# Kernel tuning notes

Hardware: AMD Instinct MI355X
Metric: run time of the kernel (lower is better)

The kernel has to match this reference:

```python
import jax, jax.numpy as jnp
import numpy as np

N = 100000      # nodes
E = 1600000     # edges
D = 64          # in_dim (node/edge feature dim)
H = 128         # hidden = 2*in_dim (num_layers=2 MLP)
OUT = 64        # out_dim
EPS = 1e-7      # GENConv eps
BN_EPS = 1e-5   # BatchNorm1d eps
NORM_EPS = 1e-12  # F.normalize eps


def setup_inputs() -> dict:
    key = jax.random.key(0)
    ks = jax.random.split(key, 10)
    feats = jax.random.normal(ks[0], (N, D), dtype=jnp.float32)
    edge_h = jax.random.normal(ks[1], (E, D), dtype=jnp.float32)
    src = jax.random.randint(ks[2], (E,), 0, N, dtype=jnp.int32)
    dst = jax.random.randint(ks[3], (E,), 0, N, dtype=jnp.int32)
    # MLP params: Linear(D,H) -> BN(H) -> ReLU -> Linear(H,OUT)
    W1 = jax.random.normal(ks[4], (D, H), dtype=jnp.float32) * 0.05
    b1 = jnp.zeros((H,), dtype=jnp.float32)
    gamma = jnp.ones((H,), dtype=jnp.float32)
    bn_beta = jnp.zeros((H,), dtype=jnp.float32)
    W2 = jax.random.normal(ks[5], (H, OUT), dtype=jnp.float32) * 0.05
    b2 = jnp.zeros((OUT,), dtype=jnp.float32)
    scale = jnp.ones((1,), dtype=jnp.float32)  # MessageNorm scale (not learned)
    return {"feats": feats, "edge_h": edge_h, "src": src, "dst": dst,
            "W1": W1, "b1": b1, "gamma": gamma, "bn_beta": bn_beta,
            "W2": W2, "b2": b2, "scale": scale}


def reference(feats, edge_h, W1, b1, gamma, bn_beta, W2, b2, scale, src, dst):
    beta = 1.0
    # message: m = relu(x_src + e) + eps            [E, D]
    m = jax.nn.relu(feats[src] + edge_h) + EPS
    # edge_softmax over incoming edges of each dst node (per feature channel)
    logits = m * beta
    gmax = jax.ops.segment_max(logits, dst, num_segments=N)   # [N, D]
    ex = jnp.exp(logits - gmax[dst])                          # [E, D]
    den = jax.ops.segment_sum(ex, dst, num_segments=N)        # [N, D]
    a = ex / den[dst]
    # weighted scatter-sum aggregation
    h = jax.ops.segment_sum(m * a, dst, num_segments=N)       # [N, D]
    # MessageNorm: feats + normalize(msg) * ||feats||_2 * scale
    feat_norm = jnp.linalg.norm(feats, axis=-1, keepdims=True)
    msg_norm = jnp.linalg.norm(h, axis=-1, keepdims=True)
    msg = h / jnp.maximum(msg_norm, NORM_EPS)
    x = feats + msg * feat_norm * scale
    # MLP: Linear -> BatchNorm1d (training-mode batch stats) -> ReLU -> Linear
    x = x @ W1 + b1
    mean = jnp.mean(x, axis=0)
    var = jnp.mean(jnp.square(x - mean), axis=0)  # biased, as torch BN
    x = (x - mean) * jax.lax.rsqrt(var + BN_EPS) * gamma + bn_beta
    x = jax.nn.relu(x)
    return x @ W2 + b2
```

## Files before the change

kernel.cpp:

```cpp
#include <hip/hip_runtime.h>
#include <cstdint>

#define N_NODES 100000
#define E_EDGES 1600000
#define D_IN 64
#define H_DIM 128
#define OUT_DIM 64
#define EPS_GEN 1e-7f
#define BN_EPS 1e-5f
#define NORM_EPS 1e-12f

#define NBUCKET 391
#define P1_CHUNK 4096

typedef int ivec4 __attribute__((ext_vector_type(4)));

__global__ __launch_bounds__(256) void hist_kernel(
    const int* __restrict__ dst, int* __restrict__ counts)
{
    int t = blockIdx.x * 256 + threadIdx.x;
    if (t < E_EDGES / 4) {
        ivec4 d = __builtin_nontemporal_load((const ivec4*)dst + t);
        atomicAdd(&counts[d.x], 1);
        atomicAdd(&counts[d.y], 1);
        atomicAdd(&counts[d.z], 1);
        atomicAdd(&counts[d.w], 1);
    }
}

__global__ __launch_bounds__(256) void scan1(
    const int* __restrict__ counts, int* __restrict__ row_start,
    int* __restrict__ bsum)
{
    __shared__ int s[256];
    int t = threadIdx.x, g = blockIdx.x * 256 + t;
    int v = (g < N_NODES) ? counts[g] : 0;
    s[t] = v;
    __syncthreads();
    #pragma unroll
    for (int off = 1; off < 256; off <<= 1) {
        int u = (t >= off) ? s[t - off] : 0;
        __syncthreads();
        s[t] += u;
        __syncthreads();
    }
    if (g < N_NODES) row_start[g] = s[t];
    if (t == 255) bsum[blockIdx.x] = s[255];
}

__global__ __launch_bounds__(512) void scan2(int* __restrict__ bsum, int nb)
{
    __shared__ int s[512];
    int t = threadIdx.x;
    int v = (t < nb) ? bsum[t] : 0;
    s[t] = v;
    __syncthreads();
    #pragma unroll
    for (int off = 1; off < 512; off <<= 1) {
        int u = (t >= off) ? s[t - off] : 0;
        __syncthreads();
        s[t] += u;
        __syncthreads();
    }
    if (t < nb) bsum[t] = s[t] - v;
}

__global__ __launch_bounds__(256) void scan3b(
    const int* __restrict__ counts, const int* __restrict__ bsum,
    int* __restrict__ row_start, int* __restrict__ bcur)
{
    int g = blockIdx.x * 256 + threadIdx.x;
    if (g < N_NODES) {
        int incl = row_start[g];
        int rs = incl - counts[g] + bsum[blockIdx.x];
        row_start[g] = rs;
        if ((g & 255) == 0) bcur[g >> 8] = rs;
    }
    if (g == 0) row_start[N_NODES] = E_EDGES;
}

__global__ __launch_bounds__(256) void bin_p1(
    const int* __restrict__ dst, const int* __restrict__ src,
    int* __restrict__ bcur, unsigned long long* __restrict__ binned)
{
    __shared__ unsigned long long buf[P1_CHUNK];
    __shared__ int cnt[NBUCKET];
    __shared__ int base_l[NBUCKET];
    __shared__ int pos[NBUCKET];
    __shared__ int gb[NBUCKET];
    __shared__ int s[256];
    int tid = threadIdx.x;
    long e0 = (long)blockIdx.x * P1_CHUNK;

    for (int b = tid; b < NBUCKET; b += 256) cnt[b] = 0;
    __syncthreads();
    for (int i = tid; i < P1_CHUNK; i += 256) {
        long e = e0 + i;
        if (e < E_EDGES) atomicAdd(&cnt[dst[e] >> 8], 1);
    }
    __syncthreads();
    int a0 = (2 * tid     < NBUCKET) ? cnt[2 * tid]     : 0;
    int a1 = (2 * tid + 1 < NBUCKET) ? cnt[2 * tid + 1] : 0;
    s[tid] = a0 + a1;
    __syncthreads();
    #pragma unroll
    for (int off = 1; off < 256; off <<= 1) {
        int u = (tid >= off) ? s[tid - off] : 0;
        __syncthreads();
        s[tid] += u;
        __syncthreads();
    }
    int pb = s[tid] - a0 - a1;
    if (2 * tid < NBUCKET)     { base_l[2 * tid] = pb;          pos[2 * tid] = pb; }
    if (2 * tid + 1 < NBUCKET) { base_l[2 * tid + 1] = pb + a0; pos[2 * tid + 1] = pb + a0; }
    __syncthreads();
    for (int i = tid; i < P1_CHUNK; i += 256) {
        long e = e0 + i;
        if (e < E_EDGES) {
            int d = dst[e], sr = src[e];
            int b = d >> 8;
            int p = atomicAdd(&pos[b], 1);
            buf[p] = ((unsigned long long)(d & 255) << 38)
                   | ((unsigned long long)(unsigned)sr << 21)
                   | (unsigned long long)e;
        }
    }
    __syncthreads();
    for (int b = tid; b < NBUCKET; b += 256) {
        int c = cnt[b];
        gb[b] = c ? atomicAdd(&bcur[b], c) : 0;
    }
    __syncthreads();
    int wv = tid >> 6, ln = tid & 63;
    for (int b = wv; b < NBUCKET; b += 4) {
        int c = cnt[b];
        if (!c) continue;
        int lb = base_l[b], g = gb[b];
        for (int i = ln; i < c; i += 64)
            binned[(size_t)g + i] = buf[lb + i];
    }
}

__global__ __launch_bounds__(256) void sort_p2(
    const unsigned long long* __restrict__ binned,
    const int* __restrict__ row_start, int2* __restrict__ adj)
{
    __shared__ int ncur[256];
    int b = blockIdx.x, tid = threadIdx.x;
    int node_base = b << 8;
    int nn = min(256, N_NODES - node_base);
    int base = row_start[node_base];
    int count = row_start[min(node_base + 256, N_NODES)] - base;
    if (tid < nn) ncur[tid] = row_start[node_base + tid] - base;
    __syncthreads();
    for (int i = tid; i < count; i += 256) {
        unsigned long long v = __builtin_nontemporal_load(&binned[(size_t)base + i]);
        int dl  = (int)(v >> 38);
        int p   = atomicAdd(&ncur[dl], 1);
        int eid = (int)(v & 0x1FFFFFull);
        int sr  = (int)((v >> 21) & 0x1FFFFull);
        adj[(size_t)base + p] = make_int2(eid, sr);
    }
}

__global__ __launch_bounds__(256) void aggregate(
    const float* __restrict__ feats, const float* __restrict__ edge_h,
    const int2* __restrict__ adj, const int* __restrict__ row_start,
    const float* __restrict__ scale, float* __restrict__ x)
{
    int node = blockIdx.x * 4 + (threadIdx.x >> 6);
    int lane = threadIdx.x & 63;
    if (node >= N_NODES) return;
    int rs = row_start[node], re = row_start[node + 1];
    float den = 0.f, hn = 0.f;

    for (int base = rs; base < re; base += 64) {
        int rem = min(64, re - base);
        int2 ad = make_int2(0, 0);
        if (base + lane < re) {
            unsigned long long v = __builtin_nontemporal_load(
                (const unsigned long long*)&adj[base + lane]);
            ad.x = (int)(unsigned)v;
            ad.y = (int)(unsigned)(v >> 32);
        }
        for (int j = 0; j < rem; j += 8) {
            #pragma unroll
            for (int u = 0; u < 8; u++) {
                int jj = j + u;
                int eid = __shfl(ad.x, jj);
                int sid = __shfl(ad.y, jj);
                float fv = feats[(size_t)sid * D_IN + lane];
                float ev = __builtin_nontemporal_load(
                               &edge_h[(size_t)eid * D_IN + lane]);
                float m = fmaxf(fv + ev, 0.f) + EPS_GEN;
                float ex = __expf(m);
                bool ok = jj < rem;
                den += ok ? ex : 0.f;
                hn  += ok ? m * ex : 0.f;
            }
        }
    }

    float h = den > 0.f ? hn / den : 0.f;
    float f = feats[(size_t)node * D_IN + lane];
    float s1 = h * h, s2 = f * f;
    #pragma unroll
    for (int off = 32; off > 0; off >>= 1) {
        s1 += __shfl_xor(s1, off, 64);
        s2 += __shfl_xor(s2, off, 64);
    }
    float xv = f + (h / fmaxf(sqrtf(s1), NORM_EPS)) * sqrtf(s2) * scale[0];
    x[(size_t)node * D_IN + lane] = xv;
}

__global__ __launch_bounds__(256) void gemm1_stats(
    const float* __restrict__ x, const float* __restrict__ W1,
    const float* __restrict__ b1, float* __restrict__ y1,
    float* __restrict__ stats)
{
    __shared__ float wlds[D_IN * H_DIM];
    __shared__ float ssum[H_DIM], ssq[H_DIM];
    int tid = threadIdx.x;
    {
        const float4* wg = (const float4*)W1;
        float4* wl = (float4*)wlds;
        #pragma unroll
        for (int i = 0; i < 8; i++) wl[tid + i * 256] = wg[tid + i * 256];
    }
    if (tid < H_DIM) { ssum[tid] = 0.f; ssq[tid] = 0.f; }
    __syncthreads();

    int rg = tid >> 5, cg = tid & 31;
    int r0 = blockIdx.x * 32 + rg * 4;
    int c0 = cg * 4;
    float acc[4][4];
    {
        float4 bb = *(const float4*)(b1 + c0);
        #pragma unroll
        for (int i = 0; i < 4; i++) {
            acc[i][0] = bb.x; acc[i][1] = bb.y; acc[i][2] = bb.z; acc[i][3] = bb.w;
        }
    }
    #pragma unroll 2
    for (int kc = 0; kc < D_IN; kc += 4) {
        float4 xr[4];
        #pragma unroll
        for (int i = 0; i < 4; i++) {
            int r = r0 + i;
            xr[i] = (r < N_NODES) ? *(const float4*)(x + (size_t)r * D_IN + kc)
                                  : make_float4(0.f, 0.f, 0.f, 0.f);
        }
        #pragma unroll
        for (int kk = 0; kk < 4; kk++) {
            float4 w4 = *(const float4*)&wlds[(kc + kk) * H_DIM + c0];
            #pragma unroll
            for (int i = 0; i < 4; i++) {
                float xv = ((const float*)&xr[i])[kk];
                acc[i][0] = fmaf(xv, w4.x, acc[i][0]);
                acc[i][1] = fmaf(xv, w4.y, acc[i][1]);
                acc[i][2] = fmaf(xv, w4.z, acc[i][2]);
                acc[i][3] = fmaf(xv, w4.w, acc[i][3]);
            }
        }
    }
    float cs[4] = {0.f, 0.f, 0.f, 0.f}, cq[4] = {0.f, 0.f, 0.f, 0.f};
    #pragma unroll
    for (int i = 0; i < 4; i++) {
        int r = r0 + i;
        if (r < N_NODES) {
            *(float4*)(y1 + (size_t)r * H_DIM + c0) =
                make_float4(acc[i][0], acc[i][1], acc[i][2], acc[i][3]);
            #pragma unroll
            for (int j = 0; j < 4; j++) {
                cs[j] += acc[i][j];
                cq[j] += acc[i][j] * acc[i][j];
            }
        }
    }
    #pragma unroll
    for (int j = 0; j < 4; j++) {
        atomicAdd(&ssum[c0 + j], cs[j]);
        atomicAdd(&ssq[c0 + j], cq[j]);
    }
    __syncthreads();
    if (tid < H_DIM) {
        unsafeAtomicAdd(&stats[tid], ssum[tid]);
        unsafeAtomicAdd(&stats[H_DIM + tid], ssq[tid]);
    }
}

__global__ __launch_bounds__(256) void gemm2_bn(
    const float* __restrict__ y1, const float* __restrict__ W2,
    const float* __restrict__ b2, const float* __restrict__ stats,
    const float* __restrict__ gamma, const float* __restrict__ beta,
    float* __restrict__ out)
{
    __shared__ float wlds[H_DIM * OUT_DIM];
    __shared__ float sc[H_DIM], sh[H_DIM];
    int tid = threadIdx.x;
    {
        const float4* wg = (const float4*)W2;
        float4* wl = (float4*)wlds;
        #pragma unroll
        for (int i = 0; i < 8; i++) wl[tid + i * 256] = wg[tid + i * 256];
    }
    if (tid < H_DIM) {
        float mean = stats[tid] * (1.f / N_NODES);
        float var  = stats[H_DIM + tid] * (1.f / N_NODES) - mean * mean;
        float rs   = rsqrtf(var + BN_EPS);
        float s    = gamma[tid] * rs;
        sc[tid] = s;
        sh[tid] = beta[tid] - mean * s;
    }
    __syncthreads();

    int rg = tid >> 4, cg = tid & 15;
    int r0 = blockIdx.x * 64 + rg * 4;
    int c0 = cg * 4;
    float acc[4][4];
    {
        float4 bb = *(const float4*)(b2 + c0);
        #pragma unroll
        for (int i = 0; i < 4; i++) {
            acc[i][0] = bb.x; acc[i][1] = bb.y; acc[i][2] = bb.z; acc[i][3] = bb.w;
        }
    }
    #pragma unroll 2
    for (int kc = 0; kc < H_DIM; kc += 4) {
        float4 sc4 = *(const float4*)&sc[kc];
        float4 sh4 = *(const float4*)&sh[kc];
        float4 yr[4];
        #pragma unroll
        for (int i = 0; i < 4; i++) {
            int r = r0 + i;
            if (r < N_NODES) {
                float4 v = *(const float4*)(y1 + (size_t)r * H_DIM + kc);
                v.x = fmaxf(fmaf(v.x, sc4.x, sh4.x), 0.f);
                v.y = fmaxf(fmaf(v.y, sc4.y, sh4.y), 0.f);
                v.z = fmaxf(fmaf(v.z, sc4.z, sh4.z), 0.f);
                v.w = fmaxf(fmaf(v.w, sc4.w, sh4.w), 0.f);
                yr[i] = v;
            } else {
                yr[i] = make_float4(0.f, 0.f, 0.f, 0.f);
            }
        }
        #pragma unroll
        for (int kk = 0; kk < 4; kk++) {
            float4 w4 = *(const float4*)&wlds[(kc + kk) * OUT_DIM + c0];
            #pragma unroll
            for (int i = 0; i < 4; i++) {
                float yv = ((const float*)&yr[i])[kk];
                acc[i][0] = fmaf(yv, w4.x, acc[i][0]);
                acc[i][1] = fmaf(yv, w4.y, acc[i][1]);
                acc[i][2] = fmaf(yv, w4.z, acc[i][2]);
                acc[i][3] = fmaf(yv, w4.w, acc[i][3]);
            }
        }
    }
    #pragma unroll
    for (int i = 0; i < 4; i++) {
        int r = r0 + i;
        if (r < N_NODES) {
            *(float4*)(out + (size_t)r * OUT_DIM + c0) =
                make_float4(acc[i][0], acc[i][1], acc[i][2], acc[i][3]);
        }
    }
}

extern "C" void kernel_launch(void* const* d_in, const int* in_sizes, int n_in,
                              void* d_out, int out_size, void* d_ws, size_t ws_size,
                              hipStream_t stream)
{
    const float* feats   = (const float*)d_in[0];
    const float* edge_h  = (const float*)d_in[1];
    const int*   src     = (const int*)d_in[2];
    const int*   dst     = (const int*)d_in[3];
    const float* W1      = (const float*)d_in[4];
    const float* b1      = (const float*)d_in[5];
    const float* gamma   = (const float*)d_in[6];
    const float* bn_beta = (const float*)d_in[7];
    const float* W2      = (const float*)d_in[8];
    const float* b2      = (const float*)d_in[9];
    const float* scale   = (const float*)d_in[10];
    float* out = (float*)d_out;

    const size_t ND = (size_t)N_NODES * D_IN;
    char* ws = (char*)d_ws;
    int*   counts    = (int*)ws;                          ws += (size_t)N_NODES * 4;
    float* stats     = (float*)ws;                        ws += 256 * 4;
    int*   bsum      = (int*)ws;                          ws += 512 * 4;
    int*   row_start = (int*)ws;                          ws += (size_t)(N_NODES + 1) * 4;
    int*   bcur      = (int*)ws;                          ws += 512 * 4;
    unsigned long long* binned = (unsigned long long*)ws; ws += (size_t)E_EDGES * 8;
    int2*  adj       = (int2*)ws;                         ws += (size_t)E_EDGES * 8;
    float* xbuf      = (float*)ws;                        ws += ND * 4;
    float* y1        = (float*)ws;

    const int NB  = (N_NODES + 255) / 256;
    const int EB4 = (E_EDGES / 4 + 255) / 256;
    const int P1B = (E_EDGES + P1_CHUNK - 1) / P1_CHUNK;

    hipMemsetAsync(counts, 0, (size_t)(N_NODES + 256) * 4, stream);

    hist_kernel<<<EB4, 256, 0, stream>>>(dst, counts);
    scan1<<<NB, 256, 0, stream>>>(counts, row_start, bsum);
    scan2<<<1, 512, 0, stream>>>(bsum, NB);
    scan3b<<<NB, 256, 0, stream>>>(counts, bsum, row_start, bcur);
    bin_p1<<<P1B, 256, 0, stream>>>(dst, src, bcur, binned);
    sort_p2<<<NBUCKET, 256, 0, stream>>>(binned, row_start, adj);
    aggregate<<<(N_NODES + 3) / 4, 256, 0, stream>>>(feats, edge_h, adj, row_start, scale, xbuf);
    gemm1_stats<<<(N_NODES + 31) / 32, 256, 0, stream>>>(xbuf, W1, b1, y1, stats);
    gemm2_bn<<<(N_NODES + 63) / 64, 256, 0, stream>>>(y1, W2, b2, stats, gamma, bn_beta, out);
}
```

Before: 887.6 us.

## Replace per-node histogram and scan with bucket-level counts, derive row starts in sort

The global per-node histogram with atomics and the three-kernel scan are replaced by a per-bucket histogram kept in shared memory plus a single small scan. Per-node row starts are now computed inside sort_p2 by a local count and scan over each bucket's binned entries. bin_p1 also loads dst and src as int4 vectors, and its write-out is reworked to use a binary search per element instead of a per-bucket wave loop. The aim is fewer launches and fewer global atomics in CSR construction, at the cost of an extra pass over binned data in sort_p2 and the binary-search overhead.

```diff
diff --git a/kernel.cpp b/kernel.cpp
--- a/kernel.cpp
+++ b/kernel.cpp
@@ -15,44 +15,33 @@
 
 typedef int ivec4 __attribute__((ext_vector_type(4)));
 
-__global__ __launch_bounds__(256) void hist_kernel(
-    const int* __restrict__ dst, int* __restrict__ counts)
-{
-    int t = blockIdx.x * 256 + threadIdx.x;
-    if (t < E_EDGES / 4) {
-        ivec4 d = __builtin_nontemporal_load((const ivec4*)dst + t);
-        atomicAdd(&counts[d.x], 1);
-        atomicAdd(&counts[d.y], 1);
-        atomicAdd(&counts[d.z], 1);
-        atomicAdd(&counts[d.w], 1);
-    }
-}
-
-__global__ __launch_bounds__(256) void scan1(
-    const int* __restrict__ counts, int* __restrict__ row_start,
-    int* __restrict__ bsum)
-{
-    __shared__ int s[256];
-    int t = threadIdx.x, g = blockIdx.x * 256 + t;
-    int v = (g < N_NODES) ? counts[g] : 0;
-    s[t] = v;
-    __syncthreads();
-    #pragma unroll
-    for (int off = 1; off < 256; off <<= 1) {
-        int u = (t >= off) ? s[t - off] : 0;
-        __syncthreads();
-        s[t] += u;
-        __syncthreads();
-    }
-    if (g < N_NODES) row_start[g] = s[t];
-    if (t == 255) bsum[blockIdx.x] = s[255];
-}
-
-__global__ __launch_bounds__(512) void scan2(int* __restrict__ bsum, int nb)
+__global__ __launch_bounds__(256) void bucket_hist(
+    const int* __restrict__ dst, int* __restrict__ bc)
+{
+    __shared__ int c[NBUCKET];
+    int tid = threadIdx.x;
+    int e0 = blockIdx.x * P1_CHUNK;
+    int total = min(P1_CHUNK, E_EDGES - e0);
+    for (int b = tid; b < NBUCKET; b += 256) c[b] = 0;
+    __syncthreads();
+    for (int i4 = tid; i4 * 4 < total; i4 += 256) {
+        ivec4 d = __builtin_nontemporal_load((const ivec4*)(dst + e0) + i4);
+        atomicAdd(&c[d.x >> 8], 1);
+        atomicAdd(&c[d.y >> 8], 1);
+        atomicAdd(&c[d.z >> 8], 1);
+        atomicAdd(&c[d.w >> 8], 1);
+    }
+    __syncthreads();
+    for (int b = tid; b < NBUCKET; b += 256)
+        if (c[b]) atomicAdd(&bc[b], c[b]);
+}
+
+__global__ __launch_bounds__(512) void bucket_scan(
+    const int* __restrict__ bc, int* __restrict__ bbase, int* __restrict__ bcur)
 {
     __shared__ int s[512];
     int t = threadIdx.x;
-    int v = (t < nb) ? bsum[t] : 0;
+    int v = (t < NBUCKET) ? bc[t] : 0;
     s[t] = v;
     __syncthreads();
     #pragma unroll
@@ -62,21 +51,12 @@
         s[t] += u;
         __syncthreads();
     }
-    if (t < nb) bsum[t] = s[t] - v;
-}
-
-__global__ __launch_bounds__(256) void scan3b(
-    const int* __restrict__ counts, const int* __restrict__ bsum,
-    int* __restrict__ row_start, int* __restrict__ bcur)
-{
-    int g = blockIdx.x * 256 + threadIdx.x;
-    if (g < N_NODES) {
-        int incl = row_start[g];
-        int rs = incl - counts[g] + bsum[blockIdx.x];
-        row_start[g] = rs;
-        if ((g & 255) == 0) bcur[g >> 8] = rs;
-    }
-    if (g == 0) row_start[N_NODES] = E_EDGES;
+    if (t < NBUCKET) {
+        int ex = s[t] - v;
+        bbase[t] = ex;
+        bcur[t]  = ex;
+    }
+    if (t == 0) bbase[NBUCKET] = E_EDGES;
 }
 
 __global__ __launch_bounds__(256) void bin_p1(
@@ -90,13 +70,17 @@
     __shared__ int gb[NBUCKET];
     __shared__ int s[256];
     int tid = threadIdx.x;
-    long e0 = (long)blockIdx.x * P1_CHUNK;
+    int e0 = blockIdx.x * P1_CHUNK;
+    int total = min(P1_CHUNK, E_EDGES - e0);
 
     for (int b = tid; b < NBUCKET; b += 256) cnt[b] = 0;
     __syncthreads();
-    for (int i = tid; i < P1_CHUNK; i += 256) {
-        long e = e0 + i;
-        if (e < E_EDGES) atomicAdd(&cnt[dst[e] >> 8], 1);
+    for (int i4 = tid; i4 * 4 < total; i4 += 256) {
+        ivec4 d = ((const ivec4*)(dst + e0))[i4];
+        atomicAdd(&cnt[d.x >> 8], 1);
+        atomicAdd(&cnt[d.y >> 8], 1);
+        atomicAdd(&cnt[d.z >> 8], 1);
+        atomicAdd(&cnt[d.w >> 8], 1);
     }
     __syncthreads();
     int a0 = (2 * tid     < NBUCKET) ? cnt[2 * tid]     : 0;
@@ -114,51 +98,77 @@
     if (2 * tid < NBUCKET)     { base_l[2 * tid] = pb;          pos[2 * tid] = pb; }
     if (2 * tid + 1 < NBUCKET) { base_l[2 * tid + 1] = pb + a0; pos[2 * tid + 1] = pb + a0; }
     __syncthreads();
-    for (int i = tid; i < P1_CHUNK; i += 256) {
-        long e = e0 + i;
-        if (e < E_EDGES) {
-            int d = dst[e], sr = src[e];
-            int b = d >> 8;
-            int p = atomicAdd(&pos[b], 1);
-            buf[p] = ((unsigned long long)(d & 255) << 38)
-                   | ((unsigned long long)(unsigned)sr << 21)
-                   | (unsigned long long)e;
-        }
-    }
-    __syncthreads();
     for (int b = tid; b < NBUCKET; b += 256) {
         int c = cnt[b];
         gb[b] = c ? atomicAdd(&bcur[b], c) : 0;
     }
     __syncthreads();
-    int wv = tid >> 6, ln = tid & 63;
-    for (int b = wv; b < NBUCKET; b += 4) {
-        int c = cnt[b];
-        if (!c) continue;
-        int lb = base_l[b], g = gb[b];
-        for (int i = ln; i < c; i += 64)
-            binned[(size_t)g + i] = buf[lb + i];
+    for (int i4 = tid; i4 * 4 < total; i4 += 256) {
+        ivec4 d  = ((const ivec4*)(dst + e0))[i4];
+        ivec4 sr = ((const ivec4*)(src + e0))[i4];
+        int e = e0 + 4 * i4;
+        #pragma unroll
+        for (int k = 0; k < 4; k++) {
+            int dd = (k == 0) ? d.x : (k == 1) ? d.y : (k == 2) ? d.z : d.w;
+            int ss = (k == 0) ? sr.x : (k == 1) ? sr.y : (k == 2) ? sr.z : sr.w;
+            int b = dd >> 8;
+            int p = atomicAdd(&pos[b], 1);
+            buf[p] = ((unsigned long long)(dd & 255) << 38)
+                   | ((unsigned long long)(unsigned)ss << 21)
+                   | (unsigned long long)(e + k);
+        }
+    }
+    __syncthreads();
+    for (int i = tid; i < total; i += 256) {
+        int lo = 0, hi = NBUCKET - 1;
+        while (lo < hi) {
+            int mid = (lo + hi + 1) >> 1;
+            if (base_l[mid] <= i) lo = mid; else hi = mid - 1;
+        }
+        binned[(size_t)gb[lo] + (i - base_l[lo])] = buf[i];
     }
 }
 
 __global__ __launch_bounds__(256) void sort_p2(
     const unsigned long long* __restrict__ binned,
-    const int* __restrict__ row_start, int2* __restrict__ adj)
-{
-    __shared__ int ncur[256];
+    const int* __restrict__ bbase, int* __restrict__ row_start,
+    int2* __restrict__ adj)
+{
+    __shared__ int lcnt[256], ncur[256];
+    __shared__ int s[256];
     int b = blockIdx.x, tid = threadIdx.x;
     int node_base = b << 8;
-    int nn = min(256, N_NODES - node_base);
-    int base = row_start[node_base];
-    int count = row_start[min(node_base + 256, N_NODES)] - base;
-    if (tid < nn) ncur[tid] = row_start[node_base + tid] - base;
+    int base  = bbase[b];
+    int count = bbase[b + 1] - base;
+    lcnt[tid] = 0;
     __syncthreads();
     for (int i = tid; i < count; i += 256) {
-        unsigned long long v = __builtin_nontemporal_load(&binned[(size_t)base + i]);
-        int dl  = (int)(v >> 38);
+        int dl = (int)(binned[(size_t)base + i] >> 38);
+        atomicAdd(&lcnt[dl], 1);
+    }
+    __syncthreads();
+    int v = lcnt[tid];
+    s[tid] = v;
+    __syncthreads();
+    #pragma unroll
+    for (int off = 1; off < 256; off <<= 1) {
+        int u = (tid >= off) ? s[tid - off] : 0;
+        __syncthreads();
+        s[tid] += u;
+        __syncthreads();
+    }
+    int excl = s[tid] - v;
+    ncur[tid] = excl;
+    int node = node_base + tid;
+    if (node < N_NODES) row_start[node] = base + excl;
+    if (b == NBUCKET - 1 && tid == 0) row_start[N_NODES] = E_EDGES;
+    __syncthreads();
+    for (int i = tid; i < count; i += 256) {
+        unsigned long long w = binned[(size_t)base + i];
+        int dl  = (int)(w >> 38);
         int p   = atomicAdd(&ncur[dl], 1);
-        int eid = (int)(v & 0x1FFFFFull);
-        int sr  = (int)((v >> 21) & 0x1FFFFull);
+        int eid = (int)(w & 0x1FFFFFull);
+        int sr  = (int)((w >> 21) & 0x1FFFFull);
         adj[(size_t)base + p] = make_int2(eid, sr);
     }
 }
@@ -386,28 +396,24 @@
 
     const size_t ND = (size_t)N_NODES * D_IN;
     char* ws = (char*)d_ws;
-    int*   counts    = (int*)ws;                          ws += (size_t)N_NODES * 4;
+    int*   bc        = (int*)ws;                          ws += 512 * 4;
     float* stats     = (float*)ws;                        ws += 256 * 4;
-    int*   bsum      = (int*)ws;                          ws += 512 * 4;
+    int*   bbase     = (int*)ws;                          ws += 512 * 4;
+    int*   bcur      = (int*)ws;                          ws += 512 * 4;
     int*   row_start = (int*)ws;                          ws += (size_t)(N_NODES + 1) * 4;
-    int*   bcur      = (int*)ws;                          ws += 512 * 4;
     unsigned long long* binned = (unsigned long long*)ws; ws += (size_t)E_EDGES * 8;
     int2*  adj       = (int2*)ws;                         ws += (size_t)E_EDGES * 8;
     float* xbuf      = (float*)ws;                        ws += ND * 4;
     float* y1        = (float*)ws;
 
-    const int NB  = (N_NODES + 255) / 256;
-    const int EB4 = (E_EDGES / 4 + 255) / 256;
     const int P1B = (E_EDGES + P1_CHUNK - 1) / P1_CHUNK;
 
-    hipMemsetAsync(counts, 0, (size_t)(N_NODES + 256) * 4, stream);
-
-    hist_kernel<<<EB4, 256, 0, stream>>>(dst, counts);
-    scan1<<<NB, 256, 0, stream>>>(counts, row_start, bsum);
-    scan2<<<1, 512, 0, stream>>>(bsum, NB);
-    scan3b<<<NB, 256, 0, stream>>>(counts, bsum, row_start, bcur);
+    hipMemsetAsync(bc, 0, (512 + 256) * 4, stream);
+
+    bucket_hist<<<P1B, 256, 0, stream>>>(dst, bc);
+    bucket_scan<<<1, 512, 0, stream>>>(bc, bbase, bcur);
     bin_p1<<<P1B, 256, 0, stream>>>(dst, src, bcur, binned);
-    sort_p2<<<NBUCKET, 256, 0, stream>>>(binned, row_start, adj);
+    sort_p2<<<NBUCKET, 256, 0, stream>>>(binned, bbase, row_start, adj);
     aggregate<<<(N_NODES + 3) / 4, 256, 0, stream>>>(feats, edge_h, adj, row_start, scale, xbuf);
     gemm1_stats<<<(N_NODES + 31) / 32, 256, 0, stream>>>(xbuf, W1, b1, y1, stats);
     gemm2_bn<<<(N_NODES + 63) / 64, 256, 0, stream>>>(y1, W2, b2, stats, gamma, bn_beta, out);
```

Result: faster. 812.7 us (-8.4%).
